# Kernel tuning notes

Measured on AMD Instinct MI355X. Metric: run time of the kernel, lower is better.

Reference implementation:

```python
import jax, jax.numpy as jnp
import numpy as np

B, T, D, H = 2048, 32, 128, 128  # batch, time steps, input_size, hidden_size


def setup_inputs() -> dict:
    key = jax.random.key(0)
    ks = jax.random.split(key, 7)
    s = 1.0 / np.sqrt(H)  # pytorch default uniform init bound
    return {
        "input_data": jax.random.normal(ks[0], (B, T - 1, D), jnp.float32),
        "W_ih": jax.random.uniform(ks[1], (4 * H, D), jnp.float32, -s, s),
        "W_hh": jax.random.uniform(ks[2], (4 * H, H), jnp.float32, -s, s),
        "b_ih": jax.random.uniform(ks[3], (4 * H,), jnp.float32, -s, s),
        "b_hh": jax.random.uniform(ks[4], (4 * H,), jnp.float32, -s, s),
        "attn_w": jax.random.uniform(ks[5], (2 * H + T - 1,), jnp.float32, -s, s),
        "attn_b": jax.random.uniform(ks[6], (1,), jnp.float32, -s, s),
    }


def reference(input_data, W_ih, W_hh, b_ih, b_hh, attn_w, attn_b):
    Bb, Tm1, Dd = input_data.shape
    Hh = W_hh.shape[1]
    # attn_linear weight acts on cat([h, c, x_series]); split it into the three parts
    w_h, w_c, w_x = attn_w[:Hh], attn_w[Hh:2 * Hh], attn_w[2 * Hh:]
    # contribution of the full per-feature time series (constant across steps): [B, D]
    x_score = jnp.einsum('btd,t->bd', input_data, w_x)

    def step(carry, x_t):
        h, c = carry  # [B, H] each
        # hidden/cell are repeated across the D input features -> scalar-per-batch shift
        score = (h @ w_h + c @ w_c + attn_b[0])[:, None] + x_score  # [B, D]
        attn = jax.nn.softmax(score, axis=1)
        wx = attn * x_t  # weighted input, [B, D]
        # single-layer LSTM cell, pytorch gate order i, f, g, o
        gates = wx @ W_ih.T + b_ih + h @ W_hh.T + b_hh  # [B, 4H]
        i_g, f_g, g_g, o_g = jnp.split(gates, 4, axis=1)
        c_new = jax.nn.sigmoid(f_g) * c + jax.nn.sigmoid(i_g) * jnp.tanh(g_g)
        h_new = jax.nn.sigmoid(o_g) * jnp.tanh(c_new)
        return (h_new, c_new), (wx, h_new)

    h0 = jnp.zeros((Bb, Hh), input_data.dtype)
    c0 = jnp.zeros((Bb, Hh), input_data.dtype)
    xs = jnp.swapaxes(input_data, 0, 1)  # [T-1, B, D]
    _, (weighted, encoded) = jax.lax.scan(step, (h0, c0), xs)
    input_weighted = jnp.swapaxes(weighted, 0, 1)  # [B, T-1, D]
    input_encoded = jnp.swapaxes(encoded, 0, 1)    # [B, T-1, H]
    return input_weighted, input_encoded
```

## Files before the change

kernel.cpp:

```cpp
#include <hip/hip_runtime.h>

#define B_   2048
#define T1_  31
#define D_   128
#define MB_  8
#define XWSZ 61440

typedef __attribute__((ext_vector_type(8))) short bf16x8;
typedef __attribute__((ext_vector_type(4))) float f32x4;
typedef __attribute__((ext_vector_type(2))) float f32x2;

#define L2E  1.4426950408889634f
#define L2E2 2.8853900817779268f

__device__ __forceinline__ unsigned cvt_pk_bf16(float lo, float hi) {
    unsigned r;
    asm("v_cvt_pk_bf16_f32 %0, %1, %2" : "=v"(r) : "v"(lo), "v"(hi));
    return r;
}
__device__ __forceinline__ float rcpf_(float x)  { return __builtin_amdgcn_rcpf(x); }
__device__ __forceinline__ float exp2f_(float x) { return __builtin_amdgcn_exp2f(x); }
__device__ __forceinline__ float sg(float xp)  { return rcpf_(1.0f + exp2f_(-xp)); }
__device__ __forceinline__ float th2(float y)  { return fmaf(-2.0f, rcpf_(1.0f + exp2f_(y)), 1.0f); }

#define BAR_LDS() asm volatile("s_waitcnt lgkmcnt(0)\n\ts_barrier" ::: "memory")

__global__ __launch_bounds__(512, 2) void enc_fused(
    const float* __restrict__ in,
    const float* __restrict__ Wih,
    const float* __restrict__ Whh,
    const float* __restrict__ bih,
    const float* __restrict__ bhh,
    const float* __restrict__ aw,
    float* __restrict__ outW,
    float* __restrict__ outE)
{
    const int tid  = threadIdx.x;
    const int lane = tid & 63;
    const int wv   = tid >> 6;
    const int b0   = blockIdx.x * MB_;
    const int l15  = lane & 15;
    const int lq   = lane >> 4;

    __shared__ __align__(16) char L[XWSZ + 4096];

    const int mg = wv;
    const int d0 = 2 * lane;
    const float* pin = in + (size_t)(b0 + mg) * (T1_ * D_) + d0;
    float2 xc[T1_];
    #pragma unroll
    for (int t = 0; t < T1_; ++t)
        xc[t] = *(const float2*)(pin + t * D_);

    bf16x8 bw[4][8];
    #pragma unroll
    for (int s = 0; s < 4; ++s) {
        const float scl = (s == 2) ? L2E2 : L2E;
        int n = s * 128 + wv * 16 + l15;
        #pragma unroll
        for (int kf = 0; kf < 8; ++kf) {
            int kb = kf * 32 + lq * 8;
            const float* wp = (kf < 4) ? (Wih + n * D_ + kb) : (Whh + n * D_ + (kb - 128));
            float4 fa = *(const float4*)(wp);
            float4 fb = *(const float4*)(wp + 4);
            union { bf16x8 v; unsigned u[4]; } tmp;
            tmp.u[0] = cvt_pk_bf16(fa.x * scl, fa.y * scl);
            tmp.u[1] = cvt_pk_bf16(fa.z * scl, fa.w * scl);
            tmp.u[2] = cvt_pk_bf16(fb.x * scl, fb.y * scl);
            tmp.u[3] = cvt_pk_bf16(fb.z * scl, fb.w * scl);
            bw[s][kf] = tmp.v;
        }
    }
    const int col = wv * 16 + l15;
    const float bsv[4] = { (bih[col]       + bhh[col])       * L2E,
                           (bih[128 + col] + bhh[128 + col]) * L2E,
                           (bih[256 + col] + bhh[256 + col]) * L2E2,
                           (bih[384 + col] + bhh[384 + col]) * L2E };

    float xs0 = 0.f, xs1 = 0.f;
    #pragma unroll
    for (int t = 0; t < T1_; ++t) {
        float wt = aw[2 * D_ + t];
        xs0 = fmaf(wt, xc[t].x, xs0);
        xs1 = fmaf(wt, xc[t].y, xs1);
    }
    float mx = fmaxf(xs0, xs1);
    #pragma unroll
    for (int o = 32; o > 0; o >>= 1) mx = fmaxf(mx, __shfl_xor(mx, o));
    float e0 = exp2f_((xs0 - mx) * L2E), e1 = exp2f_((xs1 - mx) * L2E);
    float ss = e0 + e1;
    #pragma unroll
    for (int o = 32; o > 0; o >>= 1) ss += __shfl_xor(ss, o);
    float inv = 1.0f / ss;
    const float a0 = e0 * inv;
    const float a1 = e1 * inv;

    const int wxbyte = (4 * lane) ^ (mg << 4);
    float* outWp = outW + (size_t)(b0 + mg) * (T1_ * D_) + d0;
    unsigned wx30 = 0;
    #pragma unroll
    for (int t = 0; t < T1_; ++t) {
        float w0 = a0 * xc[t].x, w1 = a1 * xc[t].y;
        f32x2 wsv; wsv[0] = w0; wsv[1] = w1;
        __builtin_nontemporal_store(wsv, (f32x2*)(outWp + t * D_));
        unsigned u = cvt_pk_bf16(w0, w1);
        if (t < 30) *(unsigned*)(L + t * 2048 + mg * 256 + wxbyte) = u;
        else        wx30 = u;
    }
    ((unsigned*)(L + XWSZ))[tid]       = 0u;
    ((unsigned*)(L + XWSZ))[tid + 512] = 0u;
    BAR_LDS();

    const int arow = l15 & 7;
    const int asw  = arow << 4;
    const char* vb[4];
    #pragma unroll
    for (int kf = 0; kf < 4; ++kf)
        vb[kf] = L + arow * 256 + ((kf * 64 + lq * 16) ^ asw);

    const int rb   = ((lane & 31) >> 4) * 4 + ((lane >> 5) << 1);
    const bool hi32 = (lane >= 32);
    const int wb0 = rb * 256       + ((2 * col) ^ (rb << 4));
    const int wb1 = (rb + 1) * 256 + ((2 * col) ^ ((rb + 1) << 4));
    float* outE0 = outE + (size_t)(b0 + rb)     * (T1_ * D_) + col;
    float* outE1 = outE + (size_t)(b0 + rb + 1) * (T1_ * D_) + col;

    float cs0 = 0.f, cs1 = 0.f;
    f32x4 accx[4];
    bf16x8 wxn[4];
    {
        bf16x8 w0[4];
        #pragma unroll
        for (int kf = 0; kf < 4; ++kf)
            w0[kf] = *(const bf16x8*)(vb[kf]);
        #pragma unroll
        for (int s = 0; s < 4; ++s) {
            float b = bsv[s];
            f32x4 aA = {b, b, b, b};
            #pragma unroll
            for (int kf = 0; kf < 4; ++kf)
                aA = __builtin_amdgcn_mfma_f32_16x16x32_bf16(w0[kf], bw[s][kf], aA, 0, 0, 0);
            accx[s] = aA;
        }
        #pragma unroll
        for (int kf = 0; kf < 4; ++kf)
            wxn[kf] = *(const bf16x8*)(vb[kf] + 2048);
    }

    #pragma unroll
    for (int t = 0; t < T1_; ++t) {
        bf16x8 hfr[4];
        #pragma unroll
        for (int kf = 0; kf < 4; ++kf)
            hfr[kf] = *(const bf16x8*)(vb[kf] + XWSZ + (t & 1) * 2048);

        f32x4 acc[4];
        #pragma unroll
        for (int s = 0; s < 4; ++s) {
            f32x4 a_ = accx[s];
            #pragma unroll
            for (int kf = 0; kf < 4; ++kf)
                a_ = __builtin_amdgcn_mfma_f32_16x16x32_bf16(hfr[kf], bw[s][4 + kf], a_, 0, 0, 0);
            acc[s] = a_;
        }

        bf16x8 wxn2[4];
        if (t < 29) {
            const int slot = (t + 2 == 30) ? 0 : (t + 2);
            #pragma unroll
            for (int kf = 0; kf < 4; ++kf)
                wxn2[kf] = *(const bf16x8*)(vb[kf] + slot * 2048);
        }
        if (t == 1)
            *(unsigned*)(L + mg * 256 + wxbyte) = wx30;

        if (t < 30) {
            #pragma unroll
            for (int s = 0; s < 4; ++s) {
                float b = bsv[s];
                f32x4 aA = {b, b, b, b};
                #pragma unroll
                for (int kf = 0; kf < 4; ++kf)
                    aA = __builtin_amdgcn_mfma_f32_16x16x32_bf16(wxn[kf], bw[s][kf], aA, 0, 0, 0);
                accx[s] = aA;
            }
        }

        float gq0[4], gq1[4];
        #pragma unroll
        for (int s = 0; s < 4; ++s) {
            gq0[s] = hi32 ? acc[s][2] : acc[s][0];
            gq1[s] = hi32 ? acc[s][3] : acc[s][1];
        }

        float si0 = sg(gq0[0]), si1 = sg(gq1[0]);
        float sf0 = sg(gq0[1]), sf1 = sg(gq1[1]);
        float tg0 = th2(gq0[2]), tg1 = th2(gq1[2]);
        float so0 = sg(gq0[3]), so1 = sg(gq1[3]);
        float cn0 = fmaf(sf0, cs0, si0 * tg0);  cs0 = cn0;
        float cn1 = fmaf(sf1, cs1, si1 * tg1);  cs1 = cn1;
        float hh0 = so0 * th2(cn0 * L2E2);
        float hh1 = so1 * th2(cn1 * L2E2);
        unsigned hu = cvt_pk_bf16(hh0, hh1);

        if (t < 30) {
            char* hw = L + XWSZ + (((t + 1) & 1) * 2048);
            *(unsigned short*)(hw + wb0) = (unsigned short)(hu & 0xffffu);
            *(unsigned short*)(hw + wb1) = (unsigned short)(hu >> 16);
        }
        __builtin_nontemporal_store(hh0, outE0 + t * D_);
        __builtin_nontemporal_store(hh1, outE1 + t * D_);

        if (t < 29) {
            #pragma unroll
            for (int kf = 0; kf < 4; ++kf) wxn[kf] = wxn2[kf];
        }

        BAR_LDS();
    }
}

extern "C" void kernel_launch(void* const* d_in, const int* in_sizes, int n_in,
                              void* d_out, int out_size, void* d_ws, size_t ws_size,
                              hipStream_t stream) {
    const float* in  = (const float*)d_in[0];
    const float* Wih = (const float*)d_in[1];
    const float* Whh = (const float*)d_in[2];
    const float* bih = (const float*)d_in[3];
    const float* bhh = (const float*)d_in[4];
    const float* aw  = (const float*)d_in[5];

    float* outW = (float*)d_out;
    float* outE = outW + (size_t)B_ * T1_ * D_;

    enc_fused<<<dim3(B_ / MB_), dim3(512), 0, stream>>>(in, Wih, Whh, bih, bhh, aw, outW, outE);
}
```

Baseline: 46.14 us.

## Split LSTM block into producer waves for input GEMM and recurrent waves

Adds a 1024-thread kernel in which eight waves compute the input-projection gate pre-activations one step ahead and stage them in double-buffered LDS, while the other eight waves run only the recurrent h·W_hh MFMAs and the gate math. The goal is to take the input GEMM off the serial per-step critical path and halve the per-wave weight register footprint. In exchange it uses 128KB of dynamic LDS per block, which limits occupancy to one block per CU, and adds an LDS round trip of the fp32 accumulators every step. The old kernel is kept as a fallback if the LDS attribute cannot be set.

```diff
diff --git a/kernel.cpp b/kernel.cpp
--- a/kernel.cpp
+++ b/kernel.cpp
@@ -4,6 +4,11 @@
 #define T1_  31
 #define D_   128
 #define MB_  8
+
+#define HB_    0
+#define AXB_   4096
+#define WXB_   69632
+#define LDS_TOT 131072
 #define XWSZ 61440
 
 typedef __attribute__((ext_vector_type(8))) short bf16x8;
@@ -25,15 +30,201 @@
 
 #define BAR_LDS() asm volatile("s_waitcnt lgkmcnt(0)\n\ts_barrier" ::: "memory")
 
+__global__ __launch_bounds__(1024, 4) void enc_split(
+    const float* __restrict__ in,  const float* __restrict__ Wih,
+    const float* __restrict__ Whh, const float* __restrict__ bih,
+    const float* __restrict__ bhh, const float* __restrict__ aw,
+    float* __restrict__ outW, float* __restrict__ outE)
+{
+    extern __shared__ char L[];
+    const int tid  = threadIdx.x;
+    const int lane = tid & 63;
+    const int wv   = tid >> 6;
+    const bool isH = (wv < 8);
+    const int cset = isH ? wv : (wv - 8);
+    const int b0   = blockIdx.x * MB_;
+    const int l15  = lane & 15;
+    const int lq   = lane >> 4;
+    const int col  = cset * 16 + l15;
+
+    bf16x8 bw[4][4];
+    #pragma unroll
+    for (int s = 0; s < 4; ++s) {
+        const float scl = (s == 2) ? L2E2 : L2E;
+        int n = s * 128 + col;
+        const float* wbase = isH ? (Whh + n * D_) : (Wih + n * D_);
+        #pragma unroll
+        for (int kf = 0; kf < 4; ++kf) {
+            const float* wp = wbase + kf * 32 + lq * 8;
+            float4 fa = *(const float4*)(wp);
+            float4 fb = *(const float4*)(wp + 4);
+            union { bf16x8 v; unsigned u[4]; } tmp;
+            tmp.u[0] = cvt_pk_bf16(fa.x * scl, fa.y * scl);
+            tmp.u[1] = cvt_pk_bf16(fa.z * scl, fa.w * scl);
+            tmp.u[2] = cvt_pk_bf16(fb.x * scl, fb.y * scl);
+            tmp.u[3] = cvt_pk_bf16(fb.z * scl, fb.w * scl);
+            bw[s][kf] = tmp.v;
+        }
+    }
+    float bsv0 = 0.f, bsv1 = 0.f, bsv2 = 0.f, bsv3 = 0.f;
+    if (!isH) {
+        bsv0 = (bih[col]       + bhh[col])       * L2E;
+        bsv1 = (bih[128 + col] + bhh[128 + col]) * L2E;
+        bsv2 = (bih[256 + col] + bhh[256 + col]) * L2E2;
+        bsv3 = (bih[384 + col] + bhh[384 + col]) * L2E;
+    }
+
+    const int mg = cset;
+    const int wxbyte = (4 * lane) ^ (mg << 4);
+    unsigned wx30 = 0;
+    if (isH) {
+        const int d0 = 2 * lane;
+        const float* pin = in + (size_t)(b0 + mg) * (T1_ * D_) + d0;
+        float2 xc[T1_];
+        #pragma unroll
+        for (int t = 0; t < T1_; ++t)
+            xc[t] = *(const float2*)(pin + t * D_);
+
+        float xs0 = 0.f, xs1 = 0.f;
+        #pragma unroll
+        for (int t = 0; t < T1_; ++t) {
+            float wt = aw[2 * D_ + t];
+            xs0 = fmaf(wt, xc[t].x, xs0);
+            xs1 = fmaf(wt, xc[t].y, xs1);
+        }
+        float mx = fmaxf(xs0, xs1);
+        #pragma unroll
+        for (int o = 32; o > 0; o >>= 1) mx = fmaxf(mx, __shfl_xor(mx, o));
+        float e0 = exp2f_((xs0 - mx) * L2E), e1 = exp2f_((xs1 - mx) * L2E);
+        float ss = e0 + e1;
+        #pragma unroll
+        for (int o = 32; o > 0; o >>= 1) ss += __shfl_xor(ss, o);
+        float inv = 1.0f / ss;
+        const float a0 = e0 * inv, a1 = e1 * inv;
+
+        float* outWp = outW + (size_t)(b0 + mg) * (T1_ * D_) + d0;
+        #pragma unroll
+        for (int t = 0; t < T1_; ++t) {
+            float w0 = a0 * xc[t].x, w1 = a1 * xc[t].y;
+            f32x2 wsv; wsv[0] = w0; wsv[1] = w1;
+            __builtin_nontemporal_store(wsv, (f32x2*)(outWp + t * D_));
+            unsigned u = cvt_pk_bf16(w0, w1);
+            if (t < 30) *(unsigned*)(L + WXB_ + t * 2048 + mg * 256 + wxbyte) = u;
+            else        wx30 = u;
+        }
+        ((unsigned*)(L + HB_))[tid]       = 0u;
+        ((unsigned*)(L + HB_))[tid + 512] = 0u;
+    }
+    BAR_LDS();
+
+    const int arow = l15 & 7;
+    const int asw  = arow << 4;
+    const char* wxv[4];  const char* hfv[4];
+    #pragma unroll
+    for (int kf = 0; kf < 4; ++kf) {
+        int fo = arow * 256 + ((kf * 64 + lq * 16) ^ asw);
+        wxv[kf] = L + WXB_ + fo;
+        hfv[kf] = L + HB_  + fo;
+    }
+    char* axp = L + AXB_ + cset * 4096 + lane * 64;
+
+    if (!isH) {
+        bf16x8 f[4];
+        #pragma unroll
+        for (int kf = 0; kf < 4; ++kf)
+            f[kf] = *(const bf16x8*)(wxv[kf]);
+        const float bs_[4] = {bsv0, bsv1, bsv2, bsv3};
+        #pragma unroll
+        for (int s = 0; s < 4; ++s) {
+            float b = bs_[s];
+            f32x4 a = {b, b, b, b};
+            #pragma unroll
+            for (int kf = 0; kf < 4; ++kf)
+                a = __builtin_amdgcn_mfma_f32_16x16x32_bf16(f[kf], bw[s][kf], a, 0, 0, 0);
+            *(f32x4*)(axp + s * 16) = a;
+        }
+    }
+    BAR_LDS();
+
+    const int rb   = ((lane & 31) >> 4) * 4 + ((lane >> 5) << 1);
+    const bool hi32 = (lane >= 32);
+    const int wb0 = rb * 256       + ((2 * col) ^ (rb << 4));
+    const int wb1 = (rb + 1) * 256 + ((2 * col) ^ ((rb + 1) << 4));
+    float* outE0 = outE + (size_t)(b0 + rb)     * (T1_ * D_) + col;
+    float* outE1 = outE + (size_t)(b0 + rb + 1) * (T1_ * D_) + col;
+    float cs0 = 0.f, cs1 = 0.f;
+
+    #pragma unroll
+    for (int t = 0; t < T1_; ++t) {
+        if (isH) {
+            f32x4 acc[4];
+            #pragma unroll
+            for (int s = 0; s < 4; ++s)
+                acc[s] = *(const f32x4*)(axp + (t & 1) * 32768 + s * 16);
+            bf16x8 hfr[4];
+            #pragma unroll
+            for (int kf = 0; kf < 4; ++kf)
+                hfr[kf] = *(const bf16x8*)(hfv[kf] + (t & 1) * 2048);
+            #pragma unroll
+            for (int s = 0; s < 4; ++s) {
+                #pragma unroll
+                for (int kf = 0; kf < 4; ++kf)
+                    acc[s] = __builtin_amdgcn_mfma_f32_16x16x32_bf16(hfr[kf], bw[s][kf], acc[s], 0, 0, 0);
+            }
+            if (t == 1)
+                *(unsigned*)(L + WXB_ + mg * 256 + wxbyte) = wx30;
+
+            float gq0[4], gq1[4];
+            #pragma unroll
+            for (int s = 0; s < 4; ++s) {
+                gq0[s] = hi32 ? acc[s][2] : acc[s][0];
+                gq1[s] = hi32 ? acc[s][3] : acc[s][1];
+            }
+            float si0 = sg(gq0[0]), si1 = sg(gq1[0]);
+            float sf0 = sg(gq0[1]), sf1 = sg(gq1[1]);
+            float tg0 = th2(gq0[2]), tg1 = th2(gq1[2]);
+            float so0 = sg(gq0[3]), so1 = sg(gq1[3]);
+            float cn0 = fmaf(sf0, cs0, si0 * tg0);  cs0 = cn0;
+            float cn1 = fmaf(sf1, cs1, si1 * tg1);  cs1 = cn1;
+            float hh0 = so0 * th2(cn0 * L2E2);
+            float hh1 = so1 * th2(cn1 * L2E2);
+            unsigned hu = cvt_pk_bf16(hh0, hh1);
+
+            if (t < 30) {
+                char* hw = L + HB_ + (((t + 1) & 1) * 2048);
+                *(unsigned short*)(hw + wb0) = (unsigned short)(hu & 0xffffu);
+                *(unsigned short*)(hw + wb1) = (unsigned short)(hu >> 16);
+            }
+            __builtin_nontemporal_store(hh0, outE0 + t * D_);
+            __builtin_nontemporal_store(hh1, outE1 + t * D_);
+        } else {
+            if (t < 30) {
+                const int slot = (t + 1 == 30) ? 0 : (t + 1);
+                bf16x8 f[4];
+                #pragma unroll
+                for (int kf = 0; kf < 4; ++kf)
+                    f[kf] = *(const bf16x8*)(wxv[kf] + slot * 2048);
+                const float bs_[4] = {bsv0, bsv1, bsv2, bsv3};
+                #pragma unroll
+                for (int s = 0; s < 4; ++s) {
+                    float b = bs_[s];
+                    f32x4 a = {b, b, b, b};
+                    #pragma unroll
+                    for (int kf = 0; kf < 4; ++kf)
+                        a = __builtin_amdgcn_mfma_f32_16x16x32_bf16(f[kf], bw[s][kf], a, 0, 0, 0);
+                    *(f32x4*)(axp + ((t + 1) & 1) * 32768 + s * 16) = a;
+                }
+            }
+        }
+        BAR_LDS();
+    }
+}
+
 __global__ __launch_bounds__(512, 2) void enc_fused(
-    const float* __restrict__ in,
-    const float* __restrict__ Wih,
-    const float* __restrict__ Whh,
-    const float* __restrict__ bih,
-    const float* __restrict__ bhh,
-    const float* __restrict__ aw,
-    float* __restrict__ outW,
-    float* __restrict__ outE)
+    const float* __restrict__ in,  const float* __restrict__ Wih,
+    const float* __restrict__ Whh, const float* __restrict__ bih,
+    const float* __restrict__ bhh, const float* __restrict__ aw,
+    float* __restrict__ outW, float* __restrict__ outE)
 {
     const int tid  = threadIdx.x;
     const int lane = tid & 63;
@@ -92,8 +283,7 @@
     #pragma unroll
     for (int o = 32; o > 0; o >>= 1) ss += __shfl_xor(ss, o);
     float inv = 1.0f / ss;
-    const float a0 = e0 * inv;
-    const float a1 = e1 * inv;
+    const float a0 = e0 * inv, a1 = e1 * inv;
 
     const int wxbyte = (4 * lane) ^ (mg << 4);
     float* outWp = outW + (size_t)(b0 + mg) * (T1_ * D_) + d0;
@@ -233,5 +423,14 @@
     float* outW = (float*)d_out;
     float* outE = outW + (size_t)B_ * T1_ * D_;
 
-    enc_fused<<<dim3(B_ / MB_), dim3(512), 0, stream>>>(in, Wih, Whh, bih, bhh, aw, outW, outE);
+    hipError_t e = hipFuncSetAttribute((const void*)enc_split,
+                                       hipFuncAttributeMaxDynamicSharedMemorySize,
+                                       LDS_TOT);
+    if (e == hipSuccess) {
+        enc_split<<<dim3(B_ / MB_), dim3(1024), LDS_TOT, stream>>>(
+            in, Wih, Whh, bih, bhh, aw, outW, outE);
+    } else {
+        enc_fused<<<dim3(B_ / MB_), dim3(512), 0, stream>>>(
+            in, Wih, Whh, bih, bhh, aw, outW, outE);
+    }
 }
```

New measurement: 65.94 us. +42.9%, slower.
